# Kernel optimization log

Hardware: AMD Instinct MI355X
Metric: run time of the kernel (lower is better)

Reference implementation:

```python
import jax, jax.numpy as jnp
import numpy as np

# LocallyConnected3D: unshared 3D conv, channels_last, valid padding, stride 1,
# linear activation, bias. Implementations 2 and 3 in the original both compute
# out[b,x,y,z,f] = sum_{i,j,k,c} in[b, x+i, y+j, z+k, c] * W[x,y,z,i,j,k,c,f] + bias[x,y,z,f]

B, X, Y, Z, CIN = 8, 32, 32, 16, 8
K = 3            # kernel_size per spatial dim
F = 16           # filters
OX, OY, OZ = X - K + 1, Y - K + 1, Z - K + 1  # 30, 30, 14 (valid, stride 1)


def setup_inputs() -> dict:
    key = jax.random.key(0)
    k1, k2 = jax.random.split(key, 2)
    inputs = jax.random.normal(k1, (B, X, Y, Z, CIN), dtype=jnp.float32)
    # glorot_uniform over the per-location receptive field
    fan_in = K * K * K * CIN
    limit = float(np.sqrt(6.0 / (fan_in + F)))
    kernel = jax.random.uniform(k2, (OX, OY, OZ, K, K, K, CIN, F),
                                dtype=jnp.float32, minval=-limit, maxval=limit)
    bias = jnp.zeros((OX, OY, OZ, F), dtype=jnp.float32)
    return {"inputs": inputs, "kernel": kernel, "bias": bias}


def _extract_patches(x):
    # (B, OX, OY, OZ, K, K, K, CIN); stride 1 valid -> plain shifted slices.
    slices = [x[:, i:i + OX, j:j + OY, k:k + OZ, :]
              for i in range(K) for j in range(K) for k in range(K)]
    p = jnp.stack(slices, axis=4)                # (B, OX, OY, OZ, K^3, CIN)
    return p.reshape(B, OX, OY, OZ, K, K, K, CIN)


def reference(inputs, kernel, bias):
    patches = _extract_patches(inputs)
    out = jnp.einsum('bxyzijkc,xyzijkcf->bxyzf', patches, kernel)
    return out + bias
```

## Files before the change

### kernel.cpp

```cpp
#include <hip/hip_runtime.h>

#define B_    8
#define OXD   30
#define OYD   30
#define OZD   14
#define NLOC  (OXD*OYD*OZD)
#define F_    16
#define T_    216
#define WPL   (T_*F_)
#define OZH   (OZD/2)
#define NBLK  (OXD*OYD*OZH)

__global__ __launch_bounds__(128, 4)
void lc3d_kernel(const float* __restrict__ in, const float* __restrict__ wgt,
                 const float* __restrict__ bias, float* __restrict__ out) {
    __shared__ float patch[B_ * 9 * 32];
    __shared__ float red[2][2 * 128];

    const int blk = blockIdx.x;
    const int ox  = blk / (OYD * OZH);
    const int rem = blk - ox * (OYD * OZH);
    const int oy  = rem / OZH;
    const int ozh = rem - oy * OZH;
    const int oz0 = 2 * ozh;
    const int loc0 = (ox * OYD + oy) * OZD + oz0;

    const int tid = threadIdx.x;
    const int fq  = tid & 3;
    const int tg  = tid >> 2;
    const float* wloc = wgt + (size_t)loc0 * WPL;

    const float bi0 = bias[(size_t)loc0 * F_ + (tid & 15)];
    const float bi1 = bias[(size_t)(loc0 + 1) * F_ + (tid & 15)];

    float4 w[14];
    #pragma unroll
    for (int l = 0; l < 2; ++l) {
        #pragma unroll
        for (int it = 0; it < 6; ++it)
            w[l * 7 + it] = *reinterpret_cast<const float4*>(
                wloc + l * WPL + (tg + 32 * it) * F_ + fq * 4);
        w[l * 7 + 6] = make_float4(0.f, 0.f, 0.f, 0.f);
        if (tg < 24)
            w[l * 7 + 6] = *reinterpret_cast<const float4*>(
                wloc + l * WPL + (tg + 192) * F_ + fq * 4);
    }

    {
        const float4* in4 = reinterpret_cast<const float4*>(in);
        float4* patch4 = reinterpret_cast<float4*>(patch);
        #pragma unroll
        for (int r = 0; r < 5; ++r) {
            int idx = tid + 128 * r;
            if (r < 4 || tid < 64) {
                int seg = idx >> 3;
                int off = idx & 7;
                int b   = seg / 9;
                int ij  = seg - b * 9;
                int i   = ij / 3;
                int j   = ij - i * 3;
                int g4  = (((b * 32 + ox + i) * 32 + (oy + j)) * 16 + oz0) * 2 + off;
                patch4[idx] = in4[g4];
            }
        }
    }
    __syncthreads();

    #pragma unroll
    for (int l = 0; l < 2; ++l) {
        float a[32];
        #pragma unroll
        for (int e = 0; e < 32; ++e) a[e] = 0.f;

        #pragma unroll
        for (int it = 0; it < 7; ++it) {
            const int t  = tg + 32 * it;
            const int tc = (t < T_) ? t : 0;
            const int vi = tc + (tc / 24) * 8 + l * 8;
            const float4 ww = w[l * 7 + it];
            #pragma unroll
            for (int b = 0; b < B_; ++b) {
                const float p = patch[b * 288 + vi];
                a[b * 4 + 0] += p * ww.x;
                a[b * 4 + 1] += p * ww.y;
                a[b * 4 + 2] += p * ww.z;
                a[b * 4 + 3] += p * ww.w;
            }
        }

#define RSTEP(m, k)                                         \
        {                                                   \
            const bool hi = (tid & (m)) != 0;               \
            _Pragma("unroll")                               \
            for (int e = 0; e < (k); ++e) {                 \
                float v = hi ? a[e] : a[e + (k)];           \
                float r = __shfl_xor(v, (m), 64);           \
                a[e] = (hi ? a[e + (k)] : a[e]) + r;        \
            }                                               \
        }
        RSTEP(4, 16)
        RSTEP(8, 8)
        RSTEP(16, 4)
        RSTEP(32, 2)
#undef RSTEP

        const int eg = ((tid & 4) << 2) | (tid & 8) | ((tid & 16) >> 2) | ((tid & 32) >> 4);
        const int wv = tid >> 6;
        red[l][wv * 128 + (eg + 0) * 4 + fq] = a[0];
        red[l][wv * 128 + (eg + 1) * 4 + fq] = a[1];
        __syncthreads();

        {
            const int b   = tid >> 4;
            const int f   = tid & 15;
            const int e2  = ((b * 4 + (f & 3)) * 4) + (f >> 2);
            const float s = (l == 0 ? bi0 : bi1) + red[l][e2] + red[l][128 + e2];
            out[((size_t)b * NLOC + loc0 + l) * F_ + f] = s;
        }
    }
}

extern "C" void kernel_launch(void* const* d_in, const int* in_sizes, int n_in,
                              void* d_out, int out_size, void* d_ws, size_t ws_size,
                              hipStream_t stream) {
    const float* in   = (const float*)d_in[0];
    const float* wgt  = (const float*)d_in[1];
    const float* bias = (const float*)d_in[2];
    float* out = (float*)d_out;
    lc3d_kernel<<<NBLK, 128, 0, stream>>>(in, wgt, bias, out);
}
```

Baseline: 38.70 us.

## Process five locations per block with register prefetch of next weights and patch

Each block now handles five consecutive output locations instead of two z-adjacent ones. While the current location is being computed, the next location's weights and input patch are loaded into registers, overlapping global loads with compute. The shared patch is compacted to hold one location, and patch index math is hoisted out of the loop. The cost is fewer blocks, extra registers for the prefetch buffers, and the lost occupancy hint from `__launch_bounds__`. The input patch is no longer shared between neighbouring z locations, so it is reloaded for each one.

```diff
diff --git a/kernel.cpp b/kernel.cpp
--- a/kernel.cpp
+++ b/kernel.cpp
@@ -8,66 +8,84 @@
 #define F_    16
 #define T_    216
 #define WPL   (T_*F_)
-#define OZH   (OZD/2)
-#define NBLK  (OXD*OYD*OZH)
+#define WPL4  (WPL/4)
+#define NQ    5
+#define NBLK  (NLOC/NQ)
 
-__global__ __launch_bounds__(128, 4)
+__global__ __launch_bounds__(128)
 void lc3d_kernel(const float* __restrict__ in, const float* __restrict__ wgt,
                  const float* __restrict__ bias, float* __restrict__ out) {
-    __shared__ float patch[B_ * 9 * 32];
+    __shared__ float patch[B_ * T_];
     __shared__ float red[2][2 * 128];
+    float4* patch4 = reinterpret_cast<float4*>(patch);
+    const float4* in4  = reinterpret_cast<const float4*>(in);
+    const float4* wgt4 = reinterpret_cast<const float4*>(wgt);
 
-    const int blk = blockIdx.x;
-    const int ox  = blk / (OYD * OZH);
-    const int rem = blk - ox * (OYD * OZH);
-    const int oy  = rem / OZH;
-    const int ozh = rem - oy * OZH;
-    const int oz0 = 2 * ozh;
-    const int loc0 = (ox * OYD + oy) * OZD + oz0;
+    const int tid  = threadIdx.x;
+    const int fq   = tid & 3;
+    const int tg   = tid >> 2;
+    const int loc0 = blockIdx.x * NQ;
 
-    const int tid = threadIdx.x;
-    const int fq  = tid & 3;
-    const int tg  = tid >> 2;
-    const float* wloc = wgt + (size_t)loc0 * WPL;
-
-    const float bi0 = bias[(size_t)loc0 * F_ + (tid & 15)];
-    const float bi1 = bias[(size_t)(loc0 + 1) * F_ + (tid & 15)];
-
-    float4 w[14];
+    int base4[4];
     #pragma unroll
-    for (int l = 0; l < 2; ++l) {
-        #pragma unroll
-        for (int it = 0; it < 6; ++it)
-            w[l * 7 + it] = *reinterpret_cast<const float4*>(
-                wloc + l * WPL + (tg + 32 * it) * F_ + fq * 4);
-        w[l * 7 + 6] = make_float4(0.f, 0.f, 0.f, 0.f);
-        if (tg < 24)
-            w[l * 7 + 6] = *reinterpret_cast<const float4*>(
-                wloc + l * WPL + (tg + 192) * F_ + fq * 4);
+    for (int r = 0; r < 4; ++r) {
+        int idx = tid + 128 * r;
+        int seg = idx / 6;
+        int off = idx - seg * 6;
+        int b   = seg / 9;
+        int ij  = seg - b * 9;
+        int i   = ij / 3;
+        int j   = ij - i * 3;
+        base4[r] = (((b * 32 + i) * 32 + j) * 16) * 2 + off;
     }
 
+    float4 w[7], p[4];
     {
-        const float4* in4 = reinterpret_cast<const float4*>(in);
-        float4* patch4 = reinterpret_cast<float4*>(patch);
+        const int loc = loc0;
+        const int ox  = loc / (OYD * OZD);
+        const int rem = loc - ox * (OYD * OZD);
+        const int oy  = rem / OZD;
+        const int oz  = rem - oy * OZD;
+        const int lo4 = ((ox * 32 + oy) * 16 + oz) * 2;
+        const float4* wl = wgt4 + (size_t)loc * WPL4 + tid;
         #pragma unroll
-        for (int r = 0; r < 5; ++r) {
-            int idx = tid + 128 * r;
-            if (r < 4 || tid < 64) {
-                int seg = idx >> 3;
-                int off = idx & 7;
-                int b   = seg / 9;
-                int ij  = seg - b * 9;
-                int i   = ij / 3;
-                int j   = ij - i * 3;
-                int g4  = (((b * 32 + ox + i) * 32 + (oy + j)) * 16 + oz0) * 2 + off;
-                patch4[idx] = in4[g4];
-            }
-        }
+        for (int it = 0; it < 6; ++it) w[it] = wl[it * 128];
+        w[6] = make_float4(0.f, 0.f, 0.f, 0.f);
+        if (tid < 96) w[6] = wl[6 * 128];
+        #pragma unroll
+        for (int r = 0; r < 3; ++r) p[r] = in4[base4[r] + lo4];
+        if (tid < 48) p[3] = in4[base4[3] + lo4];
     }
-    __syncthreads();
 
     #pragma unroll
-    for (int l = 0; l < 2; ++l) {
+    for (int q = 0; q < NQ; ++q) {
+        const int loc = loc0 + q;
+
+        #pragma unroll
+        for (int r = 0; r < 3; ++r) patch4[tid + 128 * r] = p[r];
+        if (tid < 48) patch4[tid + 384] = p[3];
+        __syncthreads();
+
+        float4 w2[7], p2[4];
+        if (q + 1 < NQ) {
+            const int nl  = loc + 1;
+            const int ox  = nl / (OYD * OZD);
+            const int rem = nl - ox * (OYD * OZD);
+            const int oy  = rem / OZD;
+            const int oz  = rem - oy * OZD;
+            const int lo4 = ((ox * 32 + oy) * 16 + oz) * 2;
+            const float4* wl = wgt4 + (size_t)nl * WPL4 + tid;
+            #pragma unroll
+            for (int it = 0; it < 6; ++it) w2[it] = wl[it * 128];
+            w2[6] = make_float4(0.f, 0.f, 0.f, 0.f);
+            if (tid < 96) w2[6] = wl[6 * 128];
+            #pragma unroll
+            for (int r = 0; r < 3; ++r) p2[r] = in4[base4[r] + lo4];
+            if (tid < 48) p2[3] = in4[base4[3] + lo4];
+        }
+
+        const float bi = bias[(size_t)loc * F_ + (tid & 15)];
+
         float a[32];
         #pragma unroll
         for (int e = 0; e < 32; ++e) a[e] = 0.f;
@@ -76,15 +94,14 @@
         for (int it = 0; it < 7; ++it) {
             const int t  = tg + 32 * it;
             const int tc = (t < T_) ? t : 0;
-            const int vi = tc + (tc / 24) * 8 + l * 8;
-            const float4 ww = w[l * 7 + it];
+            const float4 ww = w[it];
             #pragma unroll
             for (int b = 0; b < B_; ++b) {
-                const float p = patch[b * 288 + vi];
-                a[b * 4 + 0] += p * ww.x;
-                a[b * 4 + 1] += p * ww.y;
-                a[b * 4 + 2] += p * ww.z;
-                a[b * 4 + 3] += p * ww.w;
+                const float ps = patch[b * T_ + tc];
+                a[b * 4 + 0] += ps * ww.x;
+                a[b * 4 + 1] += ps * ww.y;
+                a[b * 4 + 2] += ps * ww.z;
+                a[b * 4 + 3] += ps * ww.w;
             }
         }
 
@@ -106,16 +123,23 @@
 
         const int eg = ((tid & 4) << 2) | (tid & 8) | ((tid & 16) >> 2) | ((tid & 32) >> 4);
         const int wv = tid >> 6;
-        red[l][wv * 128 + (eg + 0) * 4 + fq] = a[0];
-        red[l][wv * 128 + (eg + 1) * 4 + fq] = a[1];
+        red[q & 1][wv * 128 + (eg + 0) * 4 + fq] = a[0];
+        red[q & 1][wv * 128 + (eg + 1) * 4 + fq] = a[1];
         __syncthreads();
 
         {
-            const int b   = tid >> 4;
-            const int f   = tid & 15;
-            const int e2  = ((b * 4 + (f & 3)) * 4) + (f >> 2);
-            const float s = (l == 0 ? bi0 : bi1) + red[l][e2] + red[l][128 + e2];
-            out[((size_t)b * NLOC + loc0 + l) * F_ + f] = s;
+            const int b  = tid >> 4;
+            const int f  = tid & 15;
+            const int e2 = ((b * 4 + (f & 3)) * 4) + (f >> 2);
+            const float s = bi + red[q & 1][e2] + red[q & 1][128 + e2];
+            out[((size_t)b * NLOC + loc) * F_ + f] = s;
+        }
+
+        if (q + 1 < NQ) {
+            #pragma unroll
+            for (int it = 0; it < 7; ++it) w[it] = w2[it];
+            #pragma unroll
+            for (int r = 0; r < 4; ++r) p[r] = p2[r];
         }
     }
 }
```

Result: slower. 91.58 us (+136.6%).
